# Kernel optimization log

Hardware: AMD Instinct MI355X
Metric: run time of the kernel (lower is better)

The kernel has to match this reference:

```python
import jax, jax.numpy as jnp
import numpy as np

N, C, H, W = 32, 256, 64, 64
STRIDE = 4  # slices of refs' H dim per block, as in the torch mem_save path
EPS = 1e-12  # F.normalize clamp_min eps


def setup_inputs() -> dict:
    key = jax.random.key(0)
    k1, k2 = jax.random.split(key)
    refs = jax.random.normal(k1, (N, C, H, W), dtype=jnp.float32)
    img = jax.random.normal(k2, (C, H, W), dtype=jnp.float32)
    return {"refs": refs, "img": img}


def _l2_normalize(x, axis):
    # matches torch.nn.functional.normalize(p=2): x / max(||x||, eps)
    n = jnp.sqrt(jnp.sum(x * x, axis=axis, keepdims=True))
    return x / jnp.maximum(n, EPS)


def reference(refs, img):
    # refs: (N, C, H, W), img: (C, H, W)
    refs_n = _l2_normalize(refs, axis=1)
    img_n = _l2_normalize(img, axis=0)

    img_flat = img_n.reshape(C, H * W).T  # (HW, C) query vectors

    # group reference feature vectors by blocks of STRIDE rows of refs' H dim:
    # (N,C,H,W) -> (H, N, W, C) -> (H//STRIDE, STRIDE*N*W, C)
    blocks = refs_n.transpose(2, 0, 3, 1).reshape(H // STRIDE, STRIDE * N * W, C)

    def step(running_max, block):
        # (HW, C) x (blocksize, C)^T -> (HW, blocksize) cosine sims
        sim = jnp.einsum('xc,yc->xy', img_flat, block)
        return jnp.maximum(running_max, sim.max(axis=1)), None

    init = jnp.full((H * W,), -jnp.inf, dtype=img_flat.dtype)
    best, _ = jax.lax.scan(step, init, blocks)
    return best.reshape(H, W)
```

## Files before the change

kernel.cpp:

```cpp
#include <hip/hip_runtime.h>

#define CN 256
#define HN 64
#define WN 64
#define NNW 32
#define HW (HN*WN)
#define NREF (NNW*HW)
#define KD 256

#define BMT 256
#define BNT 64
#define NCHV 32
#define NTILES (NREF/NCHV/BNT)

using bf16x8 = __attribute__((ext_vector_type(8))) short;
using f32x4  = __attribute__((ext_vector_type(4))) float;

__device__ inline unsigned short f2bf(float x) {
  unsigned int u = __float_as_uint(x);
  return (unsigned short)((u + 0x7fffu + ((u >> 16) & 1u)) >> 16);
}

__device__ inline void atomicMaxFloat(float* addr, float val) {
  if (val >= 0.f) atomicMax(reinterpret_cast<int*>(addr), __float_as_int(val));
  else            atomicMin(reinterpret_cast<unsigned int*>(addr), __float_as_uint(val));
}

__device__ inline void gload_lds16(const void* g, void* l) {
  __builtin_amdgcn_global_load_lds(
      (const __attribute__((address_space(1))) void*)g,
      (__attribute__((address_space(3))) void*)l, 16, 0, 0);
}

__global__ __launch_bounds__(256)
void norm_kernel(const float* __restrict__ refs, const float* __restrict__ img,
                 unsigned short* __restrict__ Rb, unsigned short* __restrict__ Qb,
                 float* __restrict__ out) {
  __shared__ float tile[CN][WN + 1];
  __shared__ float ssq[4][WN];
  __shared__ float scl[WN];
  const int bid = blockIdx.x;
  const int t = threadIdx.x;
  const float* src; unsigned short* dst; int nh;
  if (bid < NNW * HN) { src = refs; dst = Rb; nh = bid; }
  else {
    src = img; dst = Qb; nh = bid - NNW * HN;
    if (t < 64) out[(size_t)nh * 64 + t] = -INFINITY;
  }
  const float* base = src + (size_t)(nh >> 6) * (CN * (size_t)HW) + (size_t)(nh & 63) * WN;

  const int c16 = t >> 4, w4 = (t & 15) * 4;
#pragma unroll
  for (int j = 0; j < 16; ++j) {
    int c = j * 16 + c16;
    float4 v = *(const float4*)&base[(size_t)c * HW + w4];
    tile[c][w4 + 0] = v.x; tile[c][w4 + 1] = v.y;
    tile[c][w4 + 2] = v.z; tile[c][w4 + 3] = v.w;
  }
  __syncthreads();
  {
    int w = t & 63, vv = t >> 6;
    float s = 0.f;
#pragma unroll 8
    for (int cc = 0; cc < 64; ++cc) { float x = tile[vv * 64 + cc][w]; s += x * x; }
    ssq[vv][w] = s;
  }
  __syncthreads();
  if (t < 64)
    scl[t] = 1.f / fmaxf(sqrtf(ssq[0][t] + ssq[1][t] + ssq[2][t] + ssq[3][t]), 1e-12f);
  __syncthreads();
  const int w = t >> 2, cq = t & 3;
  unsigned short* orow = dst + ((size_t)nh * WN + w) * KD;
  const float sc = scl[w];
#pragma unroll
  for (int j = 0; j < 8; ++j) {
    int c0 = (j * 4 + cq) * 8;
    bf16x8 o;
#pragma unroll
    for (int k = 0; k < 8; ++k) o[k] = (short)f2bf(tile[c0 + k][w] * sc);
    *(bf16x8*)&orow[c0] = o;
  }
}

#define BARR() __builtin_amdgcn_s_barrier()
#define SCHED0() __builtin_amdgcn_sched_barrier(0)
#define GATE(N) asm volatile("s_waitcnt vmcnt(" #N ")" ::: "memory")
#define LGKM0() asm volatile("s_waitcnt lgkmcnt(0)" ::: "memory")

#define STGB(P, BT) do { \
  _Pragma("unroll") \
  for (int q = 0; q < 8; ++q) \
    gload_lds16(rsb + (BT) * 16384 + q * 2048, &lds[P][wid * 4096 + q * 512]); \
} while (0)

#define STRIP(P, NI) do { \
  bf16x8 bb[8]; \
  _Pragma("unroll") \
  for (int kf = 0; kf < 8; ++kf) \
    bb[kf] = *(const bf16x8*)&lds[P][(kf >> 1) * 4096 + ((NI) * 16 + l15) * 64 \
        + ((((kf & 1) * 4 + (lane >> 4)) ^ l7) * 8)]; \
  f32x4 ac0, ac1, ac2, ac3; \
  __builtin_amdgcn_s_setprio(1); \
  _Pragma("unroll") \
  for (int kf = 0; kf < 8; ++kf) { \
    ac0 = __builtin_amdgcn_mfma_f32_16x16x32_bf16(a[0][kf], bb[kf], kf ? ac0 : ZZ, 0, 0, 0); \
    ac1 = __builtin_amdgcn_mfma_f32_16x16x32_bf16(a[1][kf], bb[kf], kf ? ac1 : ZZ, 0, 0, 0); \
    ac2 = __builtin_amdgcn_mfma_f32_16x16x32_bf16(a[2][kf], bb[kf], kf ? ac2 : ZZ, 0, 0, 0); \
    ac3 = __builtin_amdgcn_mfma_f32_16x16x32_bf16(a[3][kf], bb[kf], kf ? ac3 : ZZ, 0, 0, 0); \
  } \
  __builtin_amdgcn_s_setprio(0); \
  _Pragma("unroll") \
  for (int ee = 0; ee < 4; ++ee) { \
    run[0][ee] = fmaxf(run[0][ee], ac0[ee]); \
    run[1][ee] = fmaxf(run[1][ee], ac1[ee]); \
    run[2][ee] = fmaxf(run[2][ee], ac2[ee]); \
    run[3][ee] = fmaxf(run[3][ee], ac3[ee]); \
  } \
} while (0)

#define STRIPS(P) do { STRIP(P, 0); STRIP(P, 1); STRIP(P, 2); STRIP(P, 3); } while (0)

__global__ __launch_bounds__(256, 2)
void simmax_kernel(const unsigned short* __restrict__ Q,
                   const unsigned short* __restrict__ R,
                   float* __restrict__ out) {
  __shared__ unsigned short lds[2][16384];

  const int t = threadIdx.x;
  const int lane = t & 63;
  const int wid = t >> 6;
  const int l15 = lane & 15;
  const int l7  = lane & 7;

  const int wg  = (blockIdx.x & 7) * 64 + (blockIdx.x >> 3);
  const int nch = wg >> 4;
  const int bm  = wg & 15;

  const int srow = lane >> 3;
  const int schunk = (lane & 7) ^ srow;
  const unsigned short* rsb = R + ((size_t)nch * 4096 + srow) * KD + wid * 64 + schunk * 8;

  const f32x4 ZZ = {0.f, 0.f, 0.f, 0.f};
  f32x4 run[4];
#pragma unroll
  for (int mi = 0; mi < 4; ++mi)
#pragma unroll
    for (int ee = 0; ee < 4; ++ee) run[mi][ee] = -1e30f;

  bf16x8 a[4][8];
#pragma unroll
  for (int p = 0; p < 2; ++p) {
#pragma unroll
    for (int b = 0; b < 2; ++b) {
      const unsigned short* qsb = Q + (size_t)(bm * BMT + p * 128 + b * 64 + srow) * KD
                                    + wid * 64 + schunk * 8;
#pragma unroll
      for (int q = 0; q < 8; ++q)
        gload_lds16(qsb + q * 2048, &lds[b][wid * 4096 + q * 512]);
    }
    GATE(0); BARR(); SCHED0();
    if ((wid >> 1) == p) {
      const int b = wid & 1;
#pragma unroll
      for (int mi = 0; mi < 4; ++mi)
#pragma unroll
        for (int kf = 0; kf < 8; ++kf)
          a[mi][kf] = *(const bf16x8*)&lds[b][(kf >> 1) * 4096 + (mi * 16 + l15) * 64
              + ((((kf & 1) * 4 + (lane >> 4)) ^ l7) * 8)];
    }
    LGKM0(); BARR();
  }

  STGB(0, 0);
  for (int bt = 0; bt < NTILES - 1; ++bt) {
    STGB((bt + 1) & 1, bt + 1);
    GATE(8); BARR(); SCHED0();
    STRIPS(bt & 1);
    BARR();
  }
  GATE(0); BARR(); SCHED0();
  STRIPS((NTILES - 1) & 1);

#pragma unroll
  for (int mi = 0; mi < 4; ++mi)
#pragma unroll
    for (int ee = 0; ee < 4; ++ee) {
      float v = run[mi][ee];
      v = fmaxf(v, __shfl_xor(v, 1));
      v = fmaxf(v, __shfl_xor(v, 2));
      v = fmaxf(v, __shfl_xor(v, 4));
      v = fmaxf(v, __shfl_xor(v, 8));
      if (l15 == 0)
        atomicMaxFloat(&out[bm * BMT + wid * 64 + mi * 16 + (lane >> 4) * 4 + ee], v);
    }
}

extern "C" void kernel_launch(void* const* d_in, const int* in_sizes, int n_in,
                              void* d_out, int out_size, void* d_ws, size_t ws_size,
                              hipStream_t stream) {
  const float* refs = (const float*)d_in[0];
  const float* img  = (const float*)d_in[1];
  float* out = (float*)d_out;

  unsigned short* Rb = (unsigned short*)d_ws;
  unsigned short* Qb = Rb + (size_t)NREF * KD;

  hipLaunchKernelGGL(norm_kernel, dim3(NNW * HN + HN), dim3(256), 0, stream,
                     refs, img, Rb, Qb, out);
  hipLaunchKernelGGL(simmax_kernel, dim3(NCHV * (HW / BMT)), dim3(256), 0, stream,
                     Qb, Rb, out);
}
```

Before: 216.6 us.

## Switch simmax MFMA to 32x32x16 tiles with row-major swizzled LDS layout

Replaces the 16x16x32 bf16 MFMA tiling with 32x32x16 instructions, with each wave holding two 32-row query fragments across the full K=256. The LDS staging layout changes from K-chunked blocks to full 256-element rows with an XOR swizzle keyed on the row index, and the epilogue reduction now covers 32 lanes. The aim is fewer MFMA issues and fewer LDS B-fragment reads per output element. The trade-off is larger accumulators, which raise register pressure, and possible bank conflicts under the new swizzle.

```diff
diff --git a/kernel.cpp b/kernel.cpp
--- a/kernel.cpp
+++ b/kernel.cpp
@@ -14,7 +14,7 @@
 #define NTILES (NREF/NCHV/BNT)
 
 using bf16x8 = __attribute__((ext_vector_type(8))) short;
-using f32x4  = __attribute__((ext_vector_type(4))) float;
+using f32x16 = __attribute__((ext_vector_type(16))) float;
 
 __device__ inline unsigned short f2bf(float x) {
   unsigned int u = __float_as_uint(x);
@@ -87,38 +87,41 @@
 #define GATE(N) asm volatile("s_waitcnt vmcnt(" #N ")" ::: "memory")
 #define LGKM0() asm volatile("s_waitcnt lgkmcnt(0)" ::: "memory")
 
-#define STGB(P, BT) do { \
+#define STGW(P, BT) do { \
   _Pragma("unroll") \
   for (int q = 0; q < 8; ++q) \
-    gload_lds16(rsb + (BT) * 16384 + q * 2048, &lds[P][wid * 4096 + q * 512]); \
+    gload_lds16(rsb + (size_t)((BT) * 64 + rowq[q]) * 256 + scq[q], \
+                &lds[P][(wid * 16 + q * 2) * 256]); \
 } while (0)
 
-#define STRIP(P, NI) do { \
+#define HALFK(P, NI, H, ACM) do { \
   bf16x8 bb[8]; \
   _Pragma("unroll") \
   for (int kf = 0; kf < 8; ++kf) \
-    bb[kf] = *(const bf16x8*)&lds[P][(kf >> 1) * 4096 + ((NI) * 16 + l15) * 64 \
-        + ((((kf & 1) * 4 + (lane >> 4)) ^ l7) * 8)]; \
-  f32x4 ac0, ac1, ac2, ac3; \
+    bb[kf] = *(const bf16x8*)&lds[P][((NI) * 32 + l31) * 256 \
+        + (((((H) * 8 + kf) * 2 + hi) ^ l31) * 8)]; \
   __builtin_amdgcn_s_setprio(1); \
   _Pragma("unroll") \
   for (int kf = 0; kf < 8; ++kf) { \
-    ac0 = __builtin_amdgcn_mfma_f32_16x16x32_bf16(a[0][kf], bb[kf], kf ? ac0 : ZZ, 0, 0, 0); \
-    ac1 = __builtin_amdgcn_mfma_f32_16x16x32_bf16(a[1][kf], bb[kf], kf ? ac1 : ZZ, 0, 0, 0); \
-    ac2 = __builtin_amdgcn_mfma_f32_16x16x32_bf16(a[2][kf], bb[kf], kf ? ac2 : ZZ, 0, 0, 0); \
-    ac3 = __builtin_amdgcn_mfma_f32_16x16x32_bf16(a[3][kf], bb[kf], kf ? ac3 : ZZ, 0, 0, 0); \
+    ac0 = __builtin_amdgcn_mfma_f32_32x32x16_bf16(a[0][(H) * 8 + kf], bb[kf], \
+              ((ACM) || kf) ? ac0 : ZZ, 0, 0, 0); \
+    ac1 = __builtin_amdgcn_mfma_f32_32x32x16_bf16(a[1][(H) * 8 + kf], bb[kf], \
+              ((ACM) || kf) ? ac1 : ZZ, 0, 0, 0); \
   } \
   __builtin_amdgcn_s_setprio(0); \
-  _Pragma("unroll") \
-  for (int ee = 0; ee < 4; ++ee) { \
-    run[0][ee] = fmaxf(run[0][ee], ac0[ee]); \
-    run[1][ee] = fmaxf(run[1][ee], ac1[ee]); \
-    run[2][ee] = fmaxf(run[2][ee], ac2[ee]); \
-    run[3][ee] = fmaxf(run[3][ee], ac3[ee]); \
-  } \
 } while (0)
 
-#define STRIPS(P) do { STRIP(P, 0); STRIP(P, 1); STRIP(P, 2); STRIP(P, 3); } while (0)
+#define WINDOW(P) do { \
+  f32x16 ac0, ac1; \
+  HALFK(P, 0, 0, 0); HALFK(P, 0, 1, 1); \
+  _Pragma("unroll") \
+  for (int e = 0; e < 16; ++e) { run0[e] = fmaxf(run0[e], ac0[e]); \
+                                 run1[e] = fmaxf(run1[e], ac1[e]); } \
+  HALFK(P, 1, 0, 0); HALFK(P, 1, 1, 1); \
+  _Pragma("unroll") \
+  for (int e = 0; e < 16; ++e) { run0[e] = fmaxf(run0[e], ac0[e]); \
+                                 run1[e] = fmaxf(run1[e], ac1[e]); } \
+} while (0)
 
 __global__ __launch_bounds__(256, 2)
 void simmax_kernel(const unsigned short* __restrict__ Q,
@@ -129,69 +132,74 @@
   const int t = threadIdx.x;
   const int lane = t & 63;
   const int wid = t >> 6;
-  const int l15 = lane & 15;
-  const int l7  = lane & 7;
+  const int hi  = lane >> 5;
+  const int l31 = lane & 31;
 
   const int wg  = (blockIdx.x & 7) * 64 + (blockIdx.x >> 3);
   const int nch = wg >> 4;
   const int bm  = wg & 15;
 
-  const int srow = lane >> 3;
-  const int schunk = (lane & 7) ^ srow;
-  const unsigned short* rsb = R + ((size_t)nch * 4096 + srow) * KD + wid * 64 + schunk * 8;
-
-  const f32x4 ZZ = {0.f, 0.f, 0.f, 0.f};
-  f32x4 run[4];
-#pragma unroll
-  for (int mi = 0; mi < 4; ++mi)
-#pragma unroll
-    for (int ee = 0; ee < 4; ++ee) run[mi][ee] = -1e30f;
-
-  bf16x8 a[4][8];
+  int rowq[8], scq[8];
+#pragma unroll
+  for (int q = 0; q < 8; ++q) {
+    rowq[q] = wid * 16 + q * 2 + hi;
+    scq[q] = (l31 ^ (rowq[q] & 31)) * 8;
+  }
+  const unsigned short* rsb = R + (size_t)nch * 4096 * 256;
+
+  const f32x16 ZZ = {0,0,0,0,0,0,0,0,0,0,0,0,0,0,0,0};
+  f32x16 run0, run1;
+#pragma unroll
+  for (int e = 0; e < 16; ++e) { run0[e] = -1e30f; run1[e] = -1e30f; }
+
+  bf16x8 a[2][16];
 #pragma unroll
   for (int p = 0; p < 2; ++p) {
 #pragma unroll
     for (int b = 0; b < 2; ++b) {
-      const unsigned short* qsb = Q + (size_t)(bm * BMT + p * 128 + b * 64 + srow) * KD
-                                    + wid * 64 + schunk * 8;
+      const unsigned short* qs = Q + (size_t)(bm * BMT + p * 128 + b * 64) * 256;
 #pragma unroll
       for (int q = 0; q < 8; ++q)
-        gload_lds16(qsb + q * 2048, &lds[b][wid * 4096 + q * 512]);
+        gload_lds16(qs + (size_t)rowq[q] * 256 + scq[q],
+                    &lds[b][(wid * 16 + q * 2) * 256]);
     }
     GATE(0); BARR(); SCHED0();
     if ((wid >> 1) == p) {
       const int b = wid & 1;
 #pragma unroll
-      for (int mi = 0; mi < 4; ++mi)
-#pragma unroll
-        for (int kf = 0; kf < 8; ++kf)
-          a[mi][kf] = *(const bf16x8*)&lds[b][(kf >> 1) * 4096 + (mi * 16 + l15) * 64
-              + ((((kf & 1) * 4 + (lane >> 4)) ^ l7) * 8)];
+      for (int mi = 0; mi < 2; ++mi)
+#pragma unroll
+        for (int kf = 0; kf < 16; ++kf)
+          a[mi][kf] = *(const bf16x8*)&lds[b][(mi * 32 + l31) * 256
+              + (((kf * 2 + hi) ^ l31) * 8)];
     }
     LGKM0(); BARR();
   }
 
-  STGB(0, 0);
+  STGW(0, 0);
   for (int bt = 0; bt < NTILES - 1; ++bt) {
-    STGB((bt + 1) & 1, bt + 1);
+    STGW((bt + 1) & 1, bt + 1);
     GATE(8); BARR(); SCHED0();
-    STRIPS(bt & 1);
+    WINDOW(bt & 1);
     BARR();
   }
   GATE(0); BARR(); SCHED0();
-  STRIPS((NTILES - 1) & 1);
-
-#pragma unroll
-  for (int mi = 0; mi < 4; ++mi)
-#pragma unroll
-    for (int ee = 0; ee < 4; ++ee) {
-      float v = run[mi][ee];
+  WINDOW((NTILES - 1) & 1);
+
+#pragma unroll
+  for (int mi = 0; mi < 2; ++mi)
+#pragma unroll
+    for (int e = 0; e < 16; ++e) {
+      float v = mi ? run1[e] : run0[e];
       v = fmaxf(v, __shfl_xor(v, 1));
       v = fmaxf(v, __shfl_xor(v, 2));
       v = fmaxf(v, __shfl_xor(v, 4));
       v = fmaxf(v, __shfl_xor(v, 8));
-      if (l15 == 0)
-        atomicMaxFloat(&out[bm * BMT + wid * 64 + mi * 16 + (lane >> 4) * 4 + ee], v);
+      v = fmaxf(v, __shfl_xor(v, 16));
+      if (l31 == 0) {
+        int row = bm * BMT + wid * 64 + mi * 32 + (e & 3) + 8 * (e >> 2) + 4 * hi;
+        atomicMaxFloat(&out[row], v);
+      }
     }
 }
 
```

Result: slower. 593.4 us (+174.0%).
